# Performance work log

Hardware: AMD Instinct MI355X
Metric: run time of the kernel (lower is better)

The kernel has to match this reference:

```python
import jax, jax.numpy as jnp
import numpy as np

B, G, K = 16, 5000, 256
NUM_CELLS, HID = 100, 64
STEPS, ALPHA = 10, 0.1


def setup_inputs() -> dict:
    key = jax.random.key(0)
    ks = jax.random.split(key, 10)
    ctl = jax.random.normal(ks[0], (B, G), dtype=jnp.float32)
    drug_targets = jax.random.uniform(ks[1], (B, G), dtype=jnp.float32)
    cell_idx = jax.random.randint(ks[2], (B,), 0, NUM_CELLS)
    drug_fp = jax.random.normal(ks[3], (B, 128), dtype=jnp.float32)
    # gene->module membership matrix (constructor constant M_gk)
    M = jax.random.uniform(ks[4], (G, K), dtype=jnp.float32)
    # module-module adjacency (constructor constant A_kk), column-normalized for stability
    A = jax.random.uniform(ks[5], (K, K), dtype=jnp.float32)
    A = A / jnp.sum(A, axis=0, keepdims=True)
    # shared Dense(hidden_dim, relu): input feature dim is 3 (ctl, t, z_gene stacked)
    W1 = jax.random.normal(ks[6], (3, HID), dtype=jnp.float32) * 0.5
    b1 = jnp.zeros((HID,), dtype=jnp.float32)
    cell_emb = jax.random.normal(ks[7], (NUM_CELLS, HID), dtype=jnp.float32) * 0.05
    W2 = jax.random.normal(ks[8], (HID, 1), dtype=jnp.float32) * 0.1
    b2 = jnp.zeros((1,), dtype=jnp.float32)
    return {"ctl": ctl, "drug_targets": drug_targets, "cell_idx": cell_idx,
            "drug_fp": drug_fp, "M": M, "A": A, "W1": W1, "b1": b1,
            "cell_emb": cell_emb, "W2": W2, "b2": b2}


def reference(ctl, drug_targets, cell_idx, drug_fp, M, A, W1, b1, cell_emb, W2, b2):
    t = drug_targets                                   # [B, G]
    # max-pool gene targets into modules: max_g t[b,g] * M[g,k]
    t_mod = jnp.max(t[:, :, None] * M[None, :, :], axis=1)   # [B, K]
    # APPNP propagation: Z = (1-alpha) * Z @ A + alpha * S, fixed 10 steps
    Z = t_mod
    for _ in range(STEPS):
        Z = (1.0 - ALPHA) * (Z @ A) + ALPHA * t_mod
    z_gene = Z @ M.T                                   # [B, G]
    x = jnp.stack([ctl, t, z_gene], axis=-1)           # [B, G, 3]
    h = jax.nn.relu(x @ W1 + b1)                       # [B, G, HID]
    h = h + cell_emb[cell_idx][:, None, :]             # broadcast cell embedding
    y = jnp.squeeze(h @ W2 + b2, axis=-1)              # [B, G]
    return y
```

## Files before the change

kernel.cpp:

```cpp
#include <hip/hip_runtime.h>

#define G 5000
#define K 256
#define BATCH 16
#define HID 64
#define STEPS 10
#define NC 50
#define GPER 100

__global__ void maxpool_kernel(const float* __restrict__ t,
                               const float* __restrict__ M,
                               float* __restrict__ partials) {
    __shared__ float4 tl[GPER];
    const int c   = blockIdx.x % NC;
    const int bg  = blockIdx.x / NC;
    const int tid = threadIdx.x;
    const int g0  = c * GPER;
    const int b0  = bg * 4;

    if (tid < GPER) {
        int g = g0 + tid;
        tl[tid] = make_float4(t[(b0 + 0) * G + g], t[(b0 + 1) * G + g],
                              t[(b0 + 2) * G + g], t[(b0 + 3) * G + g]);
    }
    __syncthreads();

    float mx0 = 0.f, mx1 = 0.f, mx2 = 0.f, mx3 = 0.f;
#pragma unroll 4
    for (int gi = 0; gi < GPER; ++gi) {
        float mg = M[(size_t)(g0 + gi) * K + tid];
        float4 tv = tl[gi];
        mx0 = fmaxf(mx0, tv.x * mg);
        mx1 = fmaxf(mx1, tv.y * mg);
        mx2 = fmaxf(mx2, tv.z * mg);
        mx3 = fmaxf(mx3, tv.w * mg);
    }
    partials[((size_t)c * BATCH + b0 + 0) * K + tid] = mx0;
    partials[((size_t)c * BATCH + b0 + 1) * K + tid] = mx1;
    partials[((size_t)c * BATCH + b0 + 2) * K + tid] = mx2;
    partials[((size_t)c * BATCH + b0 + 3) * K + tid] = mx3;
}

__global__ __launch_bounds__(1024, 4)
void appnp_fused(const float* __restrict__ partials,
                 const float* __restrict__ A,
                 const int* __restrict__ cell_idx,
                 const float* __restrict__ cell_emb,
                 const float* __restrict__ W2,
                 const float* __restrict__ b2,
                 float* __restrict__ Zfin,
                 float* __restrict__ ce_dot) {
    __shared__ float4 zb[2][K / 4];
    __shared__ float  Sm[K];
    __shared__ float  red[4][K];
    __shared__ float  ce_red[HID];

    const int b  = blockIdx.x;
    const int t  = threadIdx.x;
    const int k  = t & 255;
    const int jc = t >> 8;
    const int j0 = jc * 64;

    float Areg[64];
#pragma unroll
    for (int jj = 0; jj < 64; ++jj)
        Areg[jj] = A[(size_t)(j0 + jj) * K + k];

    {
        int c0 = jc * 13, c1 = min(NC, c0 + 13);
        float m = 0.f;
        for (int c = c0; c < c1; ++c)
            m = fmaxf(m, partials[((size_t)c * BATCH + b) * K + k]);
        red[jc][k] = m;
    }
    if (t < HID) {
        int ci = cell_idx[b];
        ce_red[t] = cell_emb[ci * HID + t] * W2[t];
    }
    __syncthreads();
    if (jc == 0) {
        float s = fmaxf(fmaxf(red[0][k], red[1][k]), fmaxf(red[2][k], red[3][k]));
        Sm[k] = s;
        ((float*)zb)[k] = s;
    }
    if (t == 0) {
        float s = b2[0];
        for (int h = 0; h < HID; ++h) s += ce_red[h];
        ce_dot[b] = s;
    }
    __syncthreads();

    for (int s = 0; s < STEPS; ++s) {
        const float4* cur4 = zb[s & 1] + (j0 >> 2);
        float*        nxt  = (float*)zb[(s + 1) & 1];
        float acc = 0.f;
#pragma unroll
        for (int q = 0; q < 16; ++q) {
            float4 c4 = cur4[q];
            acc = fmaf(c4.x, Areg[4 * q + 0], acc);
            acc = fmaf(c4.y, Areg[4 * q + 1], acc);
            acc = fmaf(c4.z, Areg[4 * q + 2], acc);
            acc = fmaf(c4.w, Areg[4 * q + 3], acc);
        }
        red[jc][k] = acc;
        __syncthreads();
        if (jc == 0)
            nxt[k] = 0.9f * (red[0][k] + red[1][k] + red[2][k] + red[3][k])
                   + 0.1f * Sm[k];
        __syncthreads();
    }
    if (jc == 0) Zfin[b * K + k] = ((float*)zb)[k];
}

__global__ void final_kernel(const float* __restrict__ ctl,
                             const float* __restrict__ t_in,
                             const float* __restrict__ Z,
                             const float* __restrict__ M,
                             const float* __restrict__ W1,
                             const float* __restrict__ b1,
                             const float* __restrict__ W2,
                             const float* __restrict__ ce_dot,
                             float* __restrict__ out) {
    __shared__ float4 zl[BATCH * (K / 4)];
    __shared__ float4 wpack[HID];
    __shared__ float  w2l[HID];
    __shared__ float  cel[BATCH];

    const int t = threadIdx.x;
    const float4* Z4 = (const float4*)Z;
    for (int i = t; i < BATCH * (K / 4); i += 256) zl[i] = Z4[i];
    if (t < HID) {
        wpack[t] = make_float4(W1[t], W1[HID + t], W1[2 * HID + t], b1[t]);
        w2l[t] = W2[t];
    }
    if (t < BATCH) cel[t] = ce_dot[t];
    __syncthreads();

    const int gl = t & 63;
    const int bg = t >> 6;
    const int g = blockIdx.x * 64 + gl;
    if (g >= G) return;

    float acc[4] = {0.f, 0.f, 0.f, 0.f};
    const float4* M4 = (const float4*)(M + (size_t)g * K);
#pragma unroll 4
    for (int k4 = 0; k4 < K / 4; ++k4) {
        float4 m4 = M4[k4];
#pragma unroll
        for (int i = 0; i < 4; ++i) {
            float4 z4 = zl[(bg * 4 + i) * (K / 4) + k4];
            acc[i] = fmaf(m4.x, z4.x, acc[i]);
            acc[i] = fmaf(m4.y, z4.y, acc[i]);
            acc[i] = fmaf(m4.z, z4.z, acc[i]);
            acc[i] = fmaf(m4.w, z4.w, acc[i]);
        }
    }

    float cv[4], tv[4], y[4];
#pragma unroll
    for (int i = 0; i < 4; ++i) {
        int b = bg * 4 + i;
        cv[i] = ctl[b * G + g];
        tv[i] = t_in[b * G + g];
        y[i] = cel[b];
    }
#pragma unroll 4
    for (int h = 0; h < HID; ++h) {
        float4 w = wpack[h];
        float w2h = w2l[h];
#pragma unroll
        for (int i = 0; i < 4; ++i) {
            float pre = w.w;
            pre = fmaf(cv[i], w.x, pre);
            pre = fmaf(tv[i], w.y, pre);
            pre = fmaf(acc[i], w.z, pre);
            pre = fmaxf(pre, 0.f);
            y[i] = fmaf(pre, w2h, y[i]);
        }
    }
#pragma unroll
    for (int i = 0; i < 4; ++i)
        out[(bg * 4 + i) * G + g] = y[i];
}

extern "C" void kernel_launch(void* const* d_in, const int* in_sizes, int n_in,
                              void* d_out, int out_size, void* d_ws, size_t ws_size,
                              hipStream_t stream) {
    const float* ctl      = (const float*)d_in[0];
    const float* tgt      = (const float*)d_in[1];
    const int*   cell_idx = (const int*)d_in[2];
    const float* M        = (const float*)d_in[4];
    const float* A        = (const float*)d_in[5];
    const float* W1       = (const float*)d_in[6];
    const float* b1       = (const float*)d_in[7];
    const float* cell_emb = (const float*)d_in[8];
    const float* W2       = (const float*)d_in[9];
    const float* b2       = (const float*)d_in[10];
    float* out = (float*)d_out;

    float* partials = (float*)d_ws;
    float* Zfin = partials + (size_t)NC * BATCH * K;
    float* ce   = Zfin + BATCH * K;

    maxpool_kernel<<<NC * 4, 256, 0, stream>>>(tgt, M, partials);
    appnp_fused<<<BATCH, 1024, 0, stream>>>(partials, A, cell_idx, cell_emb,
                                            W2, b2, Zfin, ce);
    final_kernel<<<(G + 63) / 64, 256, 0, stream>>>(ctl, tgt, Zfin, M, W1, b1,
                                                    W2, ce, out);
}
```

Measured before the change: 117.2 us.

## Fuse three kernels into one cooperative kernel with grid-wide syncs

Replaces the maxpool, APPNP and final kernels with a single cooperative launch of 256 blocks of 1024 threads, using grid.sync between phases to drop launch gaps. The maxpool is re-split into 64 gene chunks with four sub-ranges per block, giving 256 partial maxima that the 16 APPNP blocks then reduce. The final phase now computes one batch row per thread rather than four, which reloads each M row 16 times instead of 4. Risks include the cost of grid-wide barriers, 240 blocks sitting idle during the propagation phase, and the cooperative launch possibly failing if 256 large blocks cannot be co-resident.

```diff
diff --git a/kernel.cpp b/kernel.cpp
--- a/kernel.cpp
+++ b/kernel.cpp
@@ -1,186 +1,178 @@
 #include <hip/hip_runtime.h>
+#include <hip/hip_cooperative_groups.h>
+namespace cg = cooperative_groups;
 
 #define G 5000
 #define K 256
 #define BATCH 16
 #define HID 64
 #define STEPS 10
-#define NC 50
-#define GPER 100
-
-__global__ void maxpool_kernel(const float* __restrict__ t,
-                               const float* __restrict__ M,
-                               float* __restrict__ partials) {
+#define NCH 64
+#define GPER 79
+#define NCP 256
+#define NBLK 256
+#define NTHR 1024
+
+__global__ __launch_bounds__(NTHR, 4)
+void fused_all(const float* __restrict__ ctl,
+               const float* __restrict__ tgt,
+               const int* __restrict__ cell_idx,
+               const float* __restrict__ M,
+               const float* __restrict__ A,
+               const float* __restrict__ W1,
+               const float* __restrict__ b1,
+               const float* __restrict__ cell_emb,
+               const float* __restrict__ W2,
+               const float* __restrict__ b2,
+               float* __restrict__ out,
+               float* __restrict__ partials,
+               float* __restrict__ Zfin,
+               float* __restrict__ ce_dot) {
+    cg::grid_group grid = cg::this_grid();
+
     __shared__ float4 tl[GPER];
-    const int c   = blockIdx.x % NC;
-    const int bg  = blockIdx.x / NC;
-    const int tid = threadIdx.x;
-    const int g0  = c * GPER;
-    const int b0  = bg * 4;
-
-    if (tid < GPER) {
-        int g = g0 + tid;
-        tl[tid] = make_float4(t[(b0 + 0) * G + g], t[(b0 + 1) * G + g],
-                              t[(b0 + 2) * G + g], t[(b0 + 3) * G + g]);
-    }
-    __syncthreads();
-
-    float mx0 = 0.f, mx1 = 0.f, mx2 = 0.f, mx3 = 0.f;
-#pragma unroll 4
-    for (int gi = 0; gi < GPER; ++gi) {
-        float mg = M[(size_t)(g0 + gi) * K + tid];
-        float4 tv = tl[gi];
-        mx0 = fmaxf(mx0, tv.x * mg);
-        mx1 = fmaxf(mx1, tv.y * mg);
-        mx2 = fmaxf(mx2, tv.z * mg);
-        mx3 = fmaxf(mx3, tv.w * mg);
-    }
-    partials[((size_t)c * BATCH + b0 + 0) * K + tid] = mx0;
-    partials[((size_t)c * BATCH + b0 + 1) * K + tid] = mx1;
-    partials[((size_t)c * BATCH + b0 + 2) * K + tid] = mx2;
-    partials[((size_t)c * BATCH + b0 + 3) * K + tid] = mx3;
-}
-
-__global__ __launch_bounds__(1024, 4)
-void appnp_fused(const float* __restrict__ partials,
-                 const float* __restrict__ A,
-                 const int* __restrict__ cell_idx,
-                 const float* __restrict__ cell_emb,
-                 const float* __restrict__ W2,
-                 const float* __restrict__ b2,
-                 float* __restrict__ Zfin,
-                 float* __restrict__ ce_dot) {
-    __shared__ float4 zb[2][K / 4];
     __shared__ float  Sm[K];
     __shared__ float  red[4][K];
     __shared__ float  ce_red[HID];
-
-    const int b  = blockIdx.x;
-    const int t  = threadIdx.x;
-    const int k  = t & 255;
-    const int jc = t >> 8;
-    const int j0 = jc * 64;
-
-    float Areg[64];
-#pragma unroll
-    for (int jj = 0; jj < 64; ++jj)
-        Areg[jj] = A[(size_t)(j0 + jj) * K + k];
-
-    {
-        int c0 = jc * 13, c1 = min(NC, c0 + 13);
-        float m = 0.f;
-        for (int c = c0; c < c1; ++c)
-            m = fmaxf(m, partials[((size_t)c * BATCH + b) * K + k]);
-        red[jc][k] = m;
-    }
-    if (t < HID) {
-        int ci = cell_idx[b];
-        ce_red[t] = cell_emb[ci * HID + t] * W2[t];
-    }
-    __syncthreads();
-    if (jc == 0) {
-        float s = fmaxf(fmaxf(red[0][k], red[1][k]), fmaxf(red[2][k], red[3][k]));
-        Sm[k] = s;
-        ((float*)zb)[k] = s;
-    }
-    if (t == 0) {
-        float s = b2[0];
-        for (int h = 0; h < HID; ++h) s += ce_red[h];
-        ce_dot[b] = s;
-    }
-    __syncthreads();
-
-    for (int s = 0; s < STEPS; ++s) {
-        const float4* cur4 = zb[s & 1] + (j0 >> 2);
-        float*        nxt  = (float*)zb[(s + 1) & 1];
-        float acc = 0.f;
-#pragma unroll
-        for (int q = 0; q < 16; ++q) {
-            float4 c4 = cur4[q];
-            acc = fmaf(c4.x, Areg[4 * q + 0], acc);
-            acc = fmaf(c4.y, Areg[4 * q + 1], acc);
-            acc = fmaf(c4.z, Areg[4 * q + 2], acc);
-            acc = fmaf(c4.w, Areg[4 * q + 3], acc);
-        }
-        red[jc][k] = acc;
-        __syncthreads();
-        if (jc == 0)
-            nxt[k] = 0.9f * (red[0][k] + red[1][k] + red[2][k] + red[3][k])
-                   + 0.1f * Sm[k];
-        __syncthreads();
-    }
-    if (jc == 0) Zfin[b * K + k] = ((float*)zb)[k];
-}
-
-__global__ void final_kernel(const float* __restrict__ ctl,
-                             const float* __restrict__ t_in,
-                             const float* __restrict__ Z,
-                             const float* __restrict__ M,
-                             const float* __restrict__ W1,
-                             const float* __restrict__ b1,
-                             const float* __restrict__ W2,
-                             const float* __restrict__ ce_dot,
-                             float* __restrict__ out) {
-    __shared__ float4 zl[BATCH * (K / 4)];
+    __shared__ float4 zb[2][K / 4];
+    __shared__ float4 zl[BATCH * (K/4)];
     __shared__ float4 wpack[HID];
     __shared__ float  w2l[HID];
-    __shared__ float  cel[BATCH];
-
-    const int t = threadIdx.x;
-    const float4* Z4 = (const float4*)Z;
-    for (int i = t; i < BATCH * (K / 4); i += 256) zl[i] = Z4[i];
-    if (t < HID) {
-        wpack[t] = make_float4(W1[t], W1[HID + t], W1[2 * HID + t], b1[t]);
-        w2l[t] = W2[t];
+
+    const int blk = blockIdx.x;
+    const int tid = threadIdx.x;
+
+    {
+        const int c   = blk >> 2;
+        const int bg  = blk & 3;
+        const int b0  = bg * 4;
+        const int g0  = c * GPER;
+        const int cnt = min(GPER, G - g0);
+        const int k   = tid & 255;
+        const int sub = tid >> 8;
+
+        if (tid < cnt) {
+            int g = g0 + tid;
+            tl[tid] = make_float4(tgt[(b0+0)*G + g], tgt[(b0+1)*G + g],
+                                  tgt[(b0+2)*G + g], tgt[(b0+3)*G + g]);
+        }
+        __syncthreads();
+
+        const int s0 = sub * 20;
+        const int s1 = min(cnt, s0 + 20);
+        float mx0 = 0.f, mx1 = 0.f, mx2 = 0.f, mx3 = 0.f;
+        for (int gi = s0; gi < s1; ++gi) {
+            float mg = M[(size_t)(g0 + gi) * K + k];
+            float4 tv = tl[gi];
+            mx0 = fmaxf(mx0, tv.x * mg);
+            mx1 = fmaxf(mx1, tv.y * mg);
+            mx2 = fmaxf(mx2, tv.z * mg);
+            mx3 = fmaxf(mx3, tv.w * mg);
+        }
+        const int cp = (c << 2) | sub;
+        partials[((size_t)cp * BATCH + b0+0) * K + k] = mx0;
+        partials[((size_t)cp * BATCH + b0+1) * K + k] = mx1;
+        partials[((size_t)cp * BATCH + b0+2) * K + k] = mx2;
+        partials[((size_t)cp * BATCH + b0+3) * K + k] = mx3;
     }
-    if (t < BATCH) cel[t] = ce_dot[t];
-    __syncthreads();
-
-    const int gl = t & 63;
-    const int bg = t >> 6;
-    const int g = blockIdx.x * 64 + gl;
-    if (g >= G) return;
-
-    float acc[4] = {0.f, 0.f, 0.f, 0.f};
-    const float4* M4 = (const float4*)(M + (size_t)g * K);
+    grid.sync();
+
+    if (blk < BATCH) {
+        const int b  = blk;
+        const int k  = tid & 255;
+        const int jc = tid >> 8;
+        const int j0 = jc * 64;
+
+        float Areg[64];
+#pragma unroll
+        for (int jj = 0; jj < 64; ++jj)
+            Areg[jj] = A[(size_t)(j0 + jj) * K + k];
+
+        {
+            float m = 0.f;
+            for (int c = j0; c < j0 + 64; ++c)
+                m = fmaxf(m, partials[((size_t)c * BATCH + b) * K + k]);
+            red[jc][k] = m;
+        }
+        if (tid < HID)
+            ce_red[tid] = cell_emb[cell_idx[b] * HID + tid] * W2[tid];
+        __syncthreads();
+        if (jc == 0) {
+            float s = fmaxf(fmaxf(red[0][k], red[1][k]),
+                            fmaxf(red[2][k], red[3][k]));
+            Sm[k] = s;
+            ((float*)zb)[k] = s;
+        }
+        if (tid == 0) {
+            float s = b2[0];
+            for (int h = 0; h < HID; ++h) s += ce_red[h];
+            ce_dot[b] = s;
+        }
+        __syncthreads();
+
+        for (int s = 0; s < STEPS; ++s) {
+            const float4* cur4 = zb[s & 1] + (j0 >> 2);
+            float*        nxt  = (float*)zb[(s + 1) & 1];
+            float acc = 0.f;
+#pragma unroll
+            for (int q = 0; q < 16; ++q) {
+                float4 c4 = cur4[q];
+                acc = fmaf(c4.x, Areg[4*q + 0], acc);
+                acc = fmaf(c4.y, Areg[4*q + 1], acc);
+                acc = fmaf(c4.z, Areg[4*q + 2], acc);
+                acc = fmaf(c4.w, Areg[4*q + 3], acc);
+            }
+            red[jc][k] = acc;
+            __syncthreads();
+            if (jc == 0)
+                nxt[k] = 0.9f * (red[0][k] + red[1][k] + red[2][k] + red[3][k])
+                       + 0.1f * Sm[k];
+            __syncthreads();
+        }
+        if (jc == 0) Zfin[b * K + k] = ((float*)zb)[k];
+    }
+    grid.sync();
+
+    if (blk < (G + 63) / 64) {
+        const float4* Z4 = (const float4*)Zfin;
+        for (int i = tid; i < BATCH * (K/4); i += NTHR) zl[i] = Z4[i];
+        if (tid < HID) {
+            wpack[tid] = make_float4(W1[tid], W1[HID + tid], W1[2*HID + tid], b1[tid]);
+            w2l[tid] = W2[tid];
+        }
+        __syncthreads();
+
+        const int gl = tid & 63;
+        const int b  = tid >> 6;
+        const int g  = blk * 64 + gl;
+        if (g < G) {
+            float acc = 0.f;
+            const float4* M4   = (const float4*)(M + (size_t)g * K);
+            const float4* zrow = &zl[b * (K/4)];
+#pragma unroll 8
+            for (int k4 = 0; k4 < K/4; ++k4) {
+                float4 m4 = M4[k4];
+                float4 z4 = zrow[k4];
+                acc = fmaf(m4.x, z4.x, acc);
+                acc = fmaf(m4.y, z4.y, acc);
+                acc = fmaf(m4.z, z4.z, acc);
+                acc = fmaf(m4.w, z4.w, acc);
+            }
+            float cv = ctl[b * G + g];
+            float tv = tgt[b * G + g];
+            float y  = ce_dot[b];
 #pragma unroll 4
-    for (int k4 = 0; k4 < K / 4; ++k4) {
-        float4 m4 = M4[k4];
-#pragma unroll
-        for (int i = 0; i < 4; ++i) {
-            float4 z4 = zl[(bg * 4 + i) * (K / 4) + k4];
-            acc[i] = fmaf(m4.x, z4.x, acc[i]);
-            acc[i] = fmaf(m4.y, z4.y, acc[i]);
-            acc[i] = fmaf(m4.z, z4.z, acc[i]);
-            acc[i] = fmaf(m4.w, z4.w, acc[i]);
+            for (int h = 0; h < HID; ++h) {
+                float4 w = wpack[h];
+                float pre = fmaf(cv, w.x, w.w);
+                pre = fmaf(tv, w.y, pre);
+                pre = fmaf(acc, w.z, pre);
+                pre = fmaxf(pre, 0.f);
+                y = fmaf(pre, w2l[h], y);
+            }
+            out[b * G + g] = y;
         }
     }
-
-    float cv[4], tv[4], y[4];
-#pragma unroll
-    for (int i = 0; i < 4; ++i) {
-        int b = bg * 4 + i;
-        cv[i] = ctl[b * G + g];
-        tv[i] = t_in[b * G + g];
-        y[i] = cel[b];
-    }
-#pragma unroll 4
-    for (int h = 0; h < HID; ++h) {
-        float4 w = wpack[h];
-        float w2h = w2l[h];
-#pragma unroll
-        for (int i = 0; i < 4; ++i) {
-            float pre = w.w;
-            pre = fmaf(cv[i], w.x, pre);
-            pre = fmaf(tv[i], w.y, pre);
-            pre = fmaf(acc[i], w.z, pre);
-            pre = fmaxf(pre, 0.f);
-            y[i] = fmaf(pre, w2h, y[i]);
-        }
-    }
-#pragma unroll
-    for (int i = 0; i < 4; ++i)
-        out[(bg * 4 + i) * G + g] = y[i];
 }
 
 extern "C" void kernel_launch(void* const* d_in, const int* in_sizes, int n_in,
@@ -199,12 +191,14 @@
     float* out = (float*)d_out;
 
     float* partials = (float*)d_ws;
-    float* Zfin = partials + (size_t)NC * BATCH * K;
-    float* ce   = Zfin + BATCH * K;
-
-    maxpool_kernel<<<NC * 4, 256, 0, stream>>>(tgt, M, partials);
-    appnp_fused<<<BATCH, 1024, 0, stream>>>(partials, A, cell_idx, cell_emb,
-                                            W2, b2, Zfin, ce);
-    final_kernel<<<(G + 63) / 64, 256, 0, stream>>>(ctl, tgt, Zfin, M, W1, b1,
-                                                    W2, ce, out);
+    float* Zfin     = partials + (size_t)NCP * BATCH * K;
+    float* ce       = Zfin + BATCH * K;
+
+    void* args[] = {
+        (void*)&ctl, (void*)&tgt, (void*)&cell_idx, (void*)&M, (void*)&A,
+        (void*)&W1, (void*)&b1, (void*)&cell_emb, (void*)&W2, (void*)&b2,
+        (void*)&out, (void*)&partials, (void*)&Zfin, (void*)&ce
+    };
+    hipLaunchCooperativeKernel((const void*)fused_all, dim3(NBLK), dim3(NTHR),
+                               args, 0, stream);
 }
```

After: 210.6 us. +79.7%, slower.

## Rebalance maxpool to 8 batches per block and prewarm A into cache

Applied to the files above, without the earlier changes.

The maxpool kernel now gives each block 40 genes and 8 batches instead of 100 genes and 4 batches. That halves how often M is reread across batch groups and raises the block count from 200 to 250. Each block also loads a slice of A and writes a dummy sum, so A should already sit in L2 when the APPNP kernel starts. The APPNP kernel's partial reduction is resized to cover 125 chunks, which makes it read more partials. The workspace gains an extra scratch buffer.

```diff
diff --git a/kernel.cpp b/kernel.cpp
--- a/kernel.cpp
+++ b/kernel.cpp
@@ -5,40 +5,47 @@
 #define BATCH 16
 #define HID 64
 #define STEPS 10
-#define NC 50
-#define GPER 100
+#define NC 125
+#define GPER 40
 
 __global__ void maxpool_kernel(const float* __restrict__ t,
                                const float* __restrict__ M,
-                               float* __restrict__ partials) {
-    __shared__ float4 tl[GPER];
-    const int c   = blockIdx.x % NC;
-    const int bg  = blockIdx.x / NC;
-    const int tid = threadIdx.x;
-    const int g0  = c * GPER;
-    const int b0  = bg * 4;
-
-    if (tid < GPER) {
-        int g = g0 + tid;
-        tl[tid] = make_float4(t[(b0 + 0) * G + g], t[(b0 + 1) * G + g],
-                              t[(b0 + 2) * G + g], t[(b0 + 3) * G + g]);
-    }
-    __syncthreads();
-
-    float mx0 = 0.f, mx1 = 0.f, mx2 = 0.f, mx3 = 0.f;
+                               const float* __restrict__ A,
+                               float* __restrict__ partials,
+                               float* __restrict__ awarm) {
+    __shared__ float tl[GPER][8];
+    const int c  = blockIdx.x >> 1;
+    const int bg = blockIdx.x & 1;
+    const int b0 = bg * 8;
+    const int k  = threadIdx.x;
+    const int g0 = c * GPER;
+
+    float4 aw = make_float4(0.f, 0.f, 0.f, 0.f);
+    if (k < 64)
+        aw = ((const float4*)A)[((size_t)blockIdx.x * 64 + k) & 16383];
+
+    for (int i = k; i < GPER * 8; i += 256) {
+        int gi = i >> 3, b = i & 7;
+        tl[gi][b] = t[(b0 + b) * G + g0 + gi];
+    }
+    __syncthreads();
+
+    float mx[8];
+#pragma unroll
+    for (int b = 0; b < 8; ++b) mx[b] = 0.f;
+
 #pragma unroll 4
     for (int gi = 0; gi < GPER; ++gi) {
-        float mg = M[(size_t)(g0 + gi) * K + tid];
-        float4 tv = tl[gi];
-        mx0 = fmaxf(mx0, tv.x * mg);
-        mx1 = fmaxf(mx1, tv.y * mg);
-        mx2 = fmaxf(mx2, tv.z * mg);
-        mx3 = fmaxf(mx3, tv.w * mg);
-    }
-    partials[((size_t)c * BATCH + b0 + 0) * K + tid] = mx0;
-    partials[((size_t)c * BATCH + b0 + 1) * K + tid] = mx1;
-    partials[((size_t)c * BATCH + b0 + 2) * K + tid] = mx2;
-    partials[((size_t)c * BATCH + b0 + 3) * K + tid] = mx3;
+        float mg = M[(size_t)(g0 + gi) * K + k];
+#pragma unroll
+        for (int b = 0; b < 8; ++b)
+            mx[b] = fmaxf(mx[b], tl[gi][b] * mg);
+    }
+#pragma unroll
+    for (int b = 0; b < 8; ++b)
+        partials[((size_t)c * BATCH + b0 + b) * K + k] = mx[b];
+
+    if (k < 64) awarm[k] = aw.x + aw.y + aw.z + aw.w;
 }
 
 __global__ __launch_bounds__(1024, 4)
@@ -67,7 +74,7 @@
         Areg[jj] = A[(size_t)(j0 + jj) * K + k];
 
     {
-        int c0 = jc * 13, c1 = min(NC, c0 + 13);
+        int c0 = jc * 32, c1 = min(NC, c0 + 32);
         float m = 0.f;
         for (int c = c0; c < c1; ++c)
             m = fmaxf(m, partials[((size_t)c * BATCH + b) * K + k]);
@@ -199,10 +206,11 @@
     float* out = (float*)d_out;
 
     float* partials = (float*)d_ws;
-    float* Zfin = partials + (size_t)NC * BATCH * K;
-    float* ce   = Zfin + BATCH * K;
-
-    maxpool_kernel<<<NC * 4, 256, 0, stream>>>(tgt, M, partials);
+    float* Zfin  = partials + (size_t)NC * BATCH * K;
+    float* ce    = Zfin + BATCH * K;
+    float* awarm = ce + BATCH;
+
+    maxpool_kernel<<<NC * 2, 256, 0, stream>>>(tgt, M, A, partials, awarm);
     appnp_fused<<<BATCH, 1024, 0, stream>>>(partials, A, cell_idx, cell_emb,
                                             W2, b2, Zfin, ce);
     final_kernel<<<(G + 63) / 64, 256, 0, stream>>>(ctl, tgt, Zfin, M, W1, b1,
```

Result: no change. 116.3 us (-0.8%).
